# Optimization experiments

Measured on AMD Instinct MI355X. Metric: run time of the kernel, lower is better.

The kernel has to match this reference:

```python
import jax, jax.numpy as jnp
import numpy as np

D = 1024        # embed_dim
NH = 16         # num_heads
DH = D // NH    # head_dim
FFN = 2048      # ffn_hidden_dim
E = 8           # num_experts
K = 2           # top_k
B, T = 2, 1024


def setup_inputs() -> dict:
    key = jax.random.key(0)
    ks = jax.random.split(key, 6)
    s = 0.02
    return {
        "x": jax.random.normal(ks[0], (B, T, D), jnp.float32),
        "ln1_g": jnp.ones((D,), jnp.float32),
        "ln1_b": jnp.zeros((D,), jnp.float32),
        "qkv_w": jax.random.normal(ks[1], (D, 3 * D), jnp.float32) * s,   # [in,out]
        "out_w": jax.random.normal(ks[2], (D, D), jnp.float32) * s,
        "ln2_g": jnp.ones((D,), jnp.float32),
        "ln2_b": jnp.zeros((D,), jnp.float32),
        "gate_w": jax.random.normal(ks[3], (D, E), jnp.float32) * s,
        "expert_biases": jnp.zeros((E,), jnp.float32),
        "w1": jax.random.normal(ks[4], (E, D, 2 * FFN), jnp.float32) * s,  # Expert.linear1 stacked
        "w2": jax.random.normal(ks[5], (E, FFN, D), jnp.float32) * s,      # Expert.linear2 stacked
    }


def _layernorm(x, g, b, eps=1e-5):
    mu = x.mean(-1, keepdims=True)
    var = ((x - mu) ** 2).mean(-1, keepdims=True)
    return (x - mu) * jax.lax.rsqrt(var + eps) * g + b


def _rope(x, theta=10000.0):
    # x: [B, T, H, Dh]; torchtune-style interleaved (even, odd) pair rotation, input_pos=None -> 0..T-1
    Tt, Dh = x.shape[1], x.shape[3]
    inv = 1.0 / (theta ** (jnp.arange(0, Dh, 2, dtype=jnp.float32) / Dh))   # [Dh/2]
    ang = jnp.arange(Tt, dtype=jnp.float32)[:, None] * inv[None, :]         # [T, Dh/2]
    cos = jnp.cos(ang)[None, :, None, :]
    sin = jnp.sin(ang)[None, :, None, :]
    x1, x2 = x[..., 0::2], x[..., 1::2]
    return jnp.stack([x1 * cos - x2 * sin, x2 * cos + x1 * sin], axis=-1).reshape(x.shape)


def reference(x, ln1_g, ln1_b, qkv_w, out_w, ln2_g, ln2_b, gate_w, expert_biases, w1, w2):
    Bx, Tx, Dx = x.shape
    # --- attention sub-block ---
    xn = _layernorm(x, ln1_g, ln1_b)
    qkv = (xn @ qkv_w).reshape(Bx, Tx, 3, NH, DH)
    q, k, v = qkv[:, :, 0], qkv[:, :, 1], qkv[:, :, 2]
    q, k = _rope(q), _rope(k)
    q = q.transpose(0, 2, 1, 3)  # [B,H,T,Dh]
    k = k.transpose(0, 2, 1, 3)
    v = v.transpose(0, 2, 1, 3)
    scores = jnp.einsum('bhqd,bhkd->bhqk', q, k) / jnp.sqrt(jnp.float32(DH))
    attn = jax.nn.softmax(scores, axis=-1)   # non-causal (SDPA default)
    o = jnp.einsum('bhqk,bhkd->bhqd', attn, v).transpose(0, 2, 1, 3).reshape(Bx, Tx, Dx)
    x = x + o @ out_w

    # --- MoE sub-block ---
    xn2 = _layernorm(x, ln2_g, ln2_b)
    gate_scores = xn2 @ gate_w + expert_biases             # [B,T,E]
    topk_vals, topk_idx = jax.lax.top_k(gate_scores, K)    # [B,T,K]
    gates = jax.nn.softmax(topk_vals, axis=-1)             # [B,T,K]
    oh = jax.nn.one_hot(topk_idx, E, dtype=x.dtype)        # [B,T,K,E]
    comb = (oh * gates[..., None]).sum(2)                  # [B,T,E] combine weights
    # dense per-expert SwiGLU FFN (equivalent to masked dispatch: unrouted weight = 0)
    h = jnp.einsum('btd,edh->beth', xn2, w1)               # [B,E,T,2*FFN]
    h1, h2 = jnp.split(h, 2, axis=-1)
    act = jax.nn.silu(h1) * h2
    eo = jnp.einsum('beth,ehd->betd', act, w2)             # [B,E,T,D]
    ffn_out = jnp.einsum('bte,betd->btd', comb, eo)
    x = x + ffn_out

    # --- load-balancing loss ---
    usage = oh.sum((0, 1, 2))                              # [E] token counts
    usage_ratio = usage / usage.sum()
    probs = jax.nn.softmax(gate_scores, axis=-1).mean((0, 1))
    prob_ratio = probs / probs.sum()
    lb_loss = (usage_ratio * prob_ratio).sum() * E
    return x, lb_loss
```

## Files before the change

kernel.cpp:

```cpp
#include <hip/hip_runtime.h>
#include <hip/hip_fp16.h>


typedef _Float16 half8 __attribute__((ext_vector_type(8)));
typedef float f32x4 __attribute__((ext_vector_type(4)));

#define DI __device__ __forceinline__

struct Desc { int e, base, rows; };

DI float blockReduceSum(float v, float* red) {
#pragma unroll
    for (int m = 32; m; m >>= 1) v += __shfl_xor(v, m);
    int w = threadIdx.x >> 6;
    if ((threadIdx.x & 63) == 0) red[w] = v;
    __syncthreads();
    v = red[0] + red[1] + red[2] + red[3];
    __syncthreads();
    return v;
}

DI void split2(float v, __half& hi, __half& lo) {
    hi = __float2half(v);
    lo = __float2half((v - __half2float(hi)) * 2048.0f);
}

enum { EPI_RESID = 0, EPI_QKV = 1 };

template<int WM, int WN, int FM, int FN, int EPI>
__global__ __launch_bounds__(256, 2)
void k_gemm_pk(const __half* __restrict__ Ah, const __half* __restrict__ Al, int lda,
               const __half* __restrict__ Bh, const __half* __restrict__ Bl, int ldb,
               float* __restrict__ Cf, int ldc, int M, int N, int K,
               const float* __restrict__ resid,
               __half* __restrict__ qh_p, __half* __restrict__ ql_p,
               __half* __restrict__ kh_p, __half* __restrict__ kl_p,
               __half* __restrict__ vth_p, __half* __restrict__ vtl_p,
               const float* __restrict__ rc, const float* __restrict__ rs)
{
    constexpr int BM = WM * FM * 16, BN = WN * FN * 16;
    constexpr int PITCH = 40;
    __shared__ __half AsH[BM * PITCH], AsL[BM * PITCH];
    __shared__ __half BsH[BN * PITCH], BsL[BN * PITCH];
    const int tid = threadIdx.x;
    const int lane = tid & 63, w = tid >> 6;
    const int l15 = lane & 15, g = lane >> 4;
    const int wm = w / WN, wn = w % WN;
    const int m0 = blockIdx.x * BM, n0 = blockIdx.y * BN;

    f32x4 acc0[FM][FN] = {}; f32x4 acc1[FM][FN] = {};

    for (int k0 = 0; k0 < K; k0 += 32) {
        __syncthreads();
#pragma unroll
        for (int it = 0; it < BM / 64; ++it) {
            int c = it * 256 + tid, row = c >> 2, kg = c & 3;
            long src = (long)(m0 + row) * lda + k0 + kg * 8;
            *(uint4*)&AsH[row * PITCH + kg * 8] = *(const uint4*)(Ah + src);
            *(uint4*)&AsL[row * PITCH + kg * 8] = *(const uint4*)(Al + src);
        }
#pragma unroll
        for (int it = 0; it < BN / 64; ++it) {
            int c = it * 256 + tid, row = c >> 2, kg = c & 3;
            long src = (long)(n0 + row) * ldb + k0 + kg * 8;
            *(uint4*)&BsH[row * PITCH + kg * 8] = *(const uint4*)(Bh + src);
            *(uint4*)&BsL[row * PITCH + kg * 8] = *(const uint4*)(Bl + src);
        }
        __syncthreads();
        half8 ah[FM], al[FM];
#pragma unroll
        for (int i = 0; i < FM; ++i) {
            int ar = (wm * FM * 16 + i * 16 + l15) * PITCH + g * 8;
            ah[i] = *(const half8*)&AsH[ar];
            al[i] = *(const half8*)&AsL[ar];
        }
#pragma unroll
        for (int n = 0; n < FN; ++n) {
            int br = (wn * FN * 16 + n * 16 + l15) * PITCH + g * 8;
            half8 bh = *(const half8*)&BsH[br];
            half8 bl = *(const half8*)&BsL[br];
#pragma unroll
            for (int i = 0; i < FM; ++i) {
                acc0[i][n] = __builtin_amdgcn_mfma_f32_16x16x32_f16(ah[i], bh, acc0[i][n], 0, 0, 0);
                acc1[i][n] = __builtin_amdgcn_mfma_f32_16x16x32_f16(ah[i], bl, acc1[i][n], 0, 0, 0);
                acc1[i][n] = __builtin_amdgcn_mfma_f32_16x16x32_f16(al[i], bh, acc1[i][n], 0, 0, 0);
            }
        }
    }

#pragma unroll
    for (int i = 0; i < FM; ++i)
#pragma unroll
    for (int n = 0; n < FN; ++n)
#pragma unroll
    for (int j = 0; j < 4; ++j) {
        float v = acc0[i][n][j] + acc1[i][n][j] * (1.0f / 2048.0f);
        int gm = m0 + wm * FM * 16 + i * 16 + g * 4 + j;
        int gn = n0 + wn * FN * 16 + n * 16 + l15;
        if constexpr (EPI == EPI_RESID) {
            Cf[(long)gm * ldc + gn] = v + resid[(long)gm * ldc + gn];
        } else {
            int t = gm & 1023, b = gm >> 10;
            float vp = __shfl_xor(v, 1);
            if (gn < 2048) {
                int col = gn & 1023;
                int i2 = (col & 63) >> 1;
                float cv = rc[t * 32 + i2], sv = rs[t * 32 + i2];
                float rot = cv * v + sv * ((lane & 1) ? vp : -vp);
                __half hi_, lo_; split2(rot, hi_, lo_);
                long o = ((long)(b * 16 + (col >> 6)) * 1024 + t) * 64 + (col & 63);
                if (gn < 1024) { qh_p[o] = hi_; ql_p[o] = lo_; }
                else           { kh_p[o] = hi_; kl_p[o] = lo_; }
            } else {
                int col = gn - 2048;
                __half hi_, lo_; split2(v, hi_, lo_);
                long o = ((long)(b * 16 + (col >> 6)) * 64 + (col & 63)) * 1024 + t;
                vth_p[o] = hi_; vtl_p[o] = lo_;
            }
        }
    }
}

__global__ __launch_bounds__(256, 2)
void k_flash(const __half* __restrict__ qh_g, const __half* __restrict__ ql_g,
             const __half* __restrict__ kh_g, const __half* __restrict__ kl_g,
             const __half* __restrict__ vth_g, const __half* __restrict__ vtl_g,
             __half* __restrict__ oh_g, __half* __restrict__ ol_g)
{
    constexpr int P = 72;
    __shared__ __half KsH[64 * P], KsL[64 * P], VsH[64 * P], VsL[64 * P], PsH[64 * P], PsL[64 * P];
    const int tid = threadIdx.x, lane = tid & 63, w = tid >> 6;
    const int l15 = lane & 15, g = lane >> 4;
    const int q0 = blockIdx.x * 64;
    const int bh = blockIdx.y;
    const long base = (long)bh * 65536;

    half8 qhi[2], qlo[2];
    {
        long qoff = base + (long)(q0 + w * 16 + l15) * 64 + g * 8;
        qhi[0] = *(const half8*)(qh_g + qoff); qhi[1] = *(const half8*)(qh_g + qoff + 32);
        qlo[0] = *(const half8*)(ql_g + qoff); qlo[1] = *(const half8*)(ql_g + qoff + 32);
    }

    float m_[4] = {-1e30f, -1e30f, -1e30f, -1e30f};
    float l_[4] = {0.f, 0.f, 0.f, 0.f};
    f32x4 o0[4] = {}, o1[4] = {};

    for (int kt = 0; kt < 16; ++kt) {
        __syncthreads();
#pragma unroll
        for (int it = 0; it < 2; ++it) {
            int c = it * 256 + tid, row = c >> 3, kg = c & 7;
            long src = base + (long)(kt * 64 + row) * 64 + kg * 8;
            *(uint4*)&KsH[row * P + kg * 8] = *(const uint4*)(kh_g + src);
            *(uint4*)&KsL[row * P + kg * 8] = *(const uint4*)(kl_g + src);
            long vs = base + (long)row * 1024 + kt * 64 + kg * 8;
            *(uint4*)&VsH[row * P + kg * 8] = *(const uint4*)(vth_g + vs);
            *(uint4*)&VsL[row * P + kg * 8] = *(const uint4*)(vtl_g + vs);
        }
        __syncthreads();

        f32x4 s0[4] = {}, s1[4] = {};
#pragma unroll
        for (int cf = 0; cf < 4; ++cf) {
            int kr = (cf * 16 + l15) * P + g * 8;
            half8 kh0 = *(const half8*)&KsH[kr], kh1 = *(const half8*)&KsH[kr + 32];
            half8 kl0 = *(const half8*)&KsL[kr], kl1 = *(const half8*)&KsL[kr + 32];
            s0[cf] = __builtin_amdgcn_mfma_f32_16x16x32_f16(qhi[0], kh0, s0[cf], 0, 0, 0);
            s1[cf] = __builtin_amdgcn_mfma_f32_16x16x32_f16(qhi[0], kl0, s1[cf], 0, 0, 0);
            s1[cf] = __builtin_amdgcn_mfma_f32_16x16x32_f16(qlo[0], kh0, s1[cf], 0, 0, 0);
            s0[cf] = __builtin_amdgcn_mfma_f32_16x16x32_f16(qhi[1], kh1, s0[cf], 0, 0, 0);
            s1[cf] = __builtin_amdgcn_mfma_f32_16x16x32_f16(qhi[1], kl1, s1[cf], 0, 0, 0);
            s1[cf] = __builtin_amdgcn_mfma_f32_16x16x32_f16(qlo[1], kh1, s1[cf], 0, 0, 0);
        }

#pragma unroll
        for (int j = 0; j < 4; ++j) {
            float sv[4];
#pragma unroll
            for (int cf = 0; cf < 4; ++cf)
                sv[cf] = (s0[cf][j] + s1[cf][j] * (1.0f / 2048.0f)) * 0.125f;
            float mx = fmaxf(fmaxf(sv[0], sv[1]), fmaxf(sv[2], sv[3]));
#pragma unroll
            for (int msk = 8; msk; msk >>= 1) mx = fmaxf(mx, __shfl_xor(mx, msk));
            float mn = fmaxf(m_[j], mx);
            float r = expf(m_[j] - mn);
            m_[j] = mn;
            float rs = 0.f;
#pragma unroll
            for (int cf = 0; cf < 4; ++cf) {
                float p = expf(sv[cf] - mn);
                rs += p;
                __half hi_, lo_; split2(p, hi_, lo_);
                PsH[(w * 16 + g * 4 + j) * P + cf * 16 + l15] = hi_;
                PsL[(w * 16 + g * 4 + j) * P + cf * 16 + l15] = lo_;
            }
#pragma unroll
            for (int msk = 8; msk; msk >>= 1) rs += __shfl_xor(rs, msk);
            l_[j] = l_[j] * r + rs;
#pragma unroll
            for (int df = 0; df < 4; ++df) { o0[df][j] *= r; o1[df][j] *= r; }
        }
        __syncthreads();

        int pr = (w * 16 + l15) * P + g * 8;
        half8 ph0 = *(const half8*)&PsH[pr], ph1 = *(const half8*)&PsH[pr + 32];
        half8 pl0 = *(const half8*)&PsL[pr], pl1 = *(const half8*)&PsL[pr + 32];
#pragma unroll
        for (int df = 0; df < 4; ++df) {
            int vr = (df * 16 + l15) * P + g * 8;
            half8 vh0 = *(const half8*)&VsH[vr], vh1 = *(const half8*)&VsH[vr + 32];
            half8 vl0 = *(const half8*)&VsL[vr], vl1 = *(const half8*)&VsL[vr + 32];
            o0[df] = __builtin_amdgcn_mfma_f32_16x16x32_f16(ph0, vh0, o0[df], 0, 0, 0);
            o1[df] = __builtin_amdgcn_mfma_f32_16x16x32_f16(ph0, vl0, o1[df], 0, 0, 0);
            o1[df] = __builtin_amdgcn_mfma_f32_16x16x32_f16(pl0, vh0, o1[df], 0, 0, 0);
            o0[df] = __builtin_amdgcn_mfma_f32_16x16x32_f16(ph1, vh1, o0[df], 0, 0, 0);
            o1[df] = __builtin_amdgcn_mfma_f32_16x16x32_f16(ph1, vl1, o1[df], 0, 0, 0);
            o1[df] = __builtin_amdgcn_mfma_f32_16x16x32_f16(pl1, vh1, o1[df], 0, 0, 0);
        }
    }

    float invl[4];
#pragma unroll
    for (int j = 0; j < 4; ++j) invl[j] = 1.0f / l_[j];
    const int b = bh >> 4, hh = bh & 15;
#pragma unroll
    for (int df = 0; df < 4; ++df)
#pragma unroll
    for (int j = 0; j < 4; ++j) {
        float v = (o0[df][j] + o1[df][j] * (1.0f / 2048.0f)) * invl[j];
        long orow = (long)b * 1024 + q0 + w * 16 + g * 4 + j;
        int col = hh * 64 + df * 16 + l15;
        __half hi_, lo_; split2(v, hi_, lo_);
        oh_g[orow * 1024 + col] = hi_;
        ol_g[orow * 1024 + col] = lo_;
    }
}

__global__ __launch_bounds__(256) void k_wconv(const float* __restrict__ src,
                                               __half* __restrict__ dst, int R, int C)
{
    src += (long)blockIdx.z * R * C;
    dst += (long)blockIdx.z * R * C;
    __shared__ float t[64][65];
    const int tid = threadIdx.x;
    const int c0 = blockIdx.x * 64, r0 = blockIdx.y * 64;
#pragma unroll
    for (int it = 0; it < 4; ++it) {
        int idx = it * 256 + tid;
        int r = idx >> 4, c4 = (idx & 15) * 4;
        float4 v = *(const float4*)(src + (long)(r0 + r) * C + c0 + c4);
        t[r][c4] = v.x; t[r][c4 + 1] = v.y; t[r][c4 + 2] = v.z; t[r][c4 + 3] = v.w;
    }
    __syncthreads();
#pragma unroll
    for (int it = 0; it < 2; ++it) {
        int idx = it * 256 + tid;
        int orow = idx >> 3, oc = (idx & 7) * 8;
        __half v[8];
#pragma unroll
        for (int j = 0; j < 8; ++j) v[j] = __float2half(t[oc + j][orow]);
        *(uint4*)(dst + (long)(c0 + orow) * R + r0 + oc) = *(uint4*)v;
    }
}

template<bool GATHER, int MODE, int FM, int FN, int WN>
__global__ __launch_bounds__(256, 2)
void k_gemm_moe(const __half* __restrict__ A, int lda, const int* __restrict__ rowidx,
                const Desc* __restrict__ desc, const int* __restrict__ ntiles,
                const __half* __restrict__ Bbase, long sB, int ldb,
                void* __restrict__ Cv, int K)
{
    if ((int)blockIdx.x >= *ntiles) return;
    Desc d = desc[blockIdx.x];
    const __half* Bp = Bbase + (long)d.e * sB;
    constexpr int WM = 4 / WN;
    constexpr int BM = WM * FM * 16, BN = WN * FN * 16;
    constexpr int PITCH = 40;
    __shared__ __half As[BM * PITCH];
    __shared__ __half Bs[BN * PITCH];
    const int tid = threadIdx.x, lane = tid & 63, w = tid >> 6;
    const int l15 = lane & 15, g = lane >> 4;
    const int wm = w / WN, wn = w % WN;
    const int n0 = blockIdx.y * (MODE == 0 ? BN / 2 : BN);

    f32x4 acc[FM][FN] = {};
    for (int k0 = 0; k0 < K; k0 += 32) {
        __syncthreads();
#pragma unroll
        for (int it = 0; it < BM / 64; ++it) {
            int c = it * 256 + tid, row = c >> 2, kg = c & 3;
            uint4 v = make_uint4(0, 0, 0, 0);
            if constexpr (GATHER) {
                if (row < d.rows) {
                    int ar = rowidx[d.base + row];
                    v = *(const uint4*)(A + (long)ar * lda + k0 + kg * 8);
                }
            } else {
                v = *(const uint4*)(A + (long)(d.base + row) * lda + k0 + kg * 8);
            }
            *(uint4*)&As[row * PITCH + kg * 8] = v;
        }
#pragma unroll
        for (int it = 0; it < BN / 64; ++it) {
            int c = it * 256 + tid, row = c >> 2, kg = c & 3;
            int srcrow;
            if constexpr (MODE == 0) {
                int pb = row >> 4, w4 = row & 15;
                srcrow = ((pb & 1) ? 2048 : 0) + n0 + (pb >> 1) * 16 + w4;
            } else {
                srcrow = n0 + row;
            }
            *(uint4*)&Bs[row * PITCH + kg * 8] =
                *(const uint4*)(Bp + (long)srcrow * ldb + k0 + kg * 8);
        }
        __syncthreads();
        half8 a[FM];
#pragma unroll
        for (int i = 0; i < FM; ++i)
            a[i] = *(const half8*)&As[(wm * FM * 16 + i * 16 + l15) * PITCH + g * 8];
#pragma unroll
        for (int n = 0; n < FN; ++n) {
            half8 b = *(const half8*)&Bs[(wn * FN * 16 + n * 16 + l15) * PITCH + g * 8];
#pragma unroll
            for (int i = 0; i < FM; ++i)
                acc[i][n] = __builtin_amdgcn_mfma_f32_16x16x32_f16(a[i], b, acc[i][n], 0, 0, 0);
        }
    }

    if constexpr (MODE == 0) {
#pragma unroll
        for (int i = 0; i < FM; ++i)
#pragma unroll
        for (int p = 0; p < FN / 2; ++p)
#pragma unroll
        for (int j = 0; j < 4; ++j) {
            int rl = wm * FM * 16 + i * 16 + g * 4 + j;
            float h1 = acc[i][2 * p][j], h2 = acc[i][2 * p + 1][j];
            float a = h1 / (1.0f + expf(-h1)) * h2;
            if (rl >= d.rows) a = 0.0f;
            int jc = n0 + wn * (FN * 8) + p * 16 + l15;
            ((__half*)Cv)[(long)(d.base + rl) * 2048 + jc] = __float2half(a);
        }
    } else {
#pragma unroll
        for (int i = 0; i < FM; ++i)
#pragma unroll
        for (int n = 0; n < FN; ++n)
#pragma unroll
        for (int j = 0; j < 4; ++j) {
            int rl = wm * FM * 16 + i * 16 + g * 4 + j;
            int gn = n0 + wn * FN * 16 + n * 16 + l15;
            ((float*)Cv)[(long)(d.base + rl) * 1024 + gn] = acc[i][n][j];
        }
    }
}

__global__ __launch_bounds__(256) void k_transpose_pk(const float* __restrict__ src,
    __half* __restrict__ dsth, __half* __restrict__ dstl, int R, int C)
{
    __shared__ float t[64][65];
    const int tid = threadIdx.x;
    const int c0 = blockIdx.x * 64, r0 = blockIdx.y * 64;
#pragma unroll
    for (int it = 0; it < 4; ++it) {
        int idx = it * 256 + tid;
        int r = idx >> 4, c4 = (idx & 15) * 4;
        float4 v = *(const float4*)(src + (long)(r0 + r) * C + c0 + c4);
        t[r][c4] = v.x; t[r][c4 + 1] = v.y; t[r][c4 + 2] = v.z; t[r][c4 + 3] = v.w;
    }
    __syncthreads();
#pragma unroll
    for (int it = 0; it < 4; ++it) {
        int idx = it * 256 + tid;
        int orow = idx >> 4, oc = (idx & 15) * 4;
        __half hs[4], ls[4];
#pragma unroll
        for (int m = 0; m < 4; ++m) split2(t[oc + m][orow], hs[m], ls[m]);
        long o = (long)(c0 + orow) * R + r0 + oc;
        *(uint2*)&dsth[o] = *(uint2*)hs;
        *(uint2*)&dstl[o] = *(uint2*)ls;
    }
}

template<int MODE>
__global__ __launch_bounds__(256) void k_ln(const float* __restrict__ X,
    const float* __restrict__ g, const float* __restrict__ bta,
    void* __restrict__ o1, void* __restrict__ o2)
{
    __shared__ float red[4];
    const long row = blockIdx.x;
    const float* xr = X + row * 1024;
    const int c = threadIdx.x * 4;
    float4 v = *(const float4*)(xr + c);
    float mu = blockReduceSum(v.x + v.y + v.z + v.w, red) * (1.0f / 1024.0f);
    float d0 = v.x - mu, d1 = v.y - mu, d2 = v.z - mu, d3 = v.w - mu;
    float var = blockReduceSum(d0 * d0 + d1 * d1 + d2 * d2 + d3 * d3, red) * (1.0f / 1024.0f);
    float rs = 1.0f / sqrtf(var + 1e-5f);
    float4 gv = *(const float4*)(g + c);
    float4 bv = *(const float4*)(bta + c);
    float y[4] = {d0 * rs * gv.x + bv.x, d1 * rs * gv.y + bv.y,
                  d2 * rs * gv.z + bv.z, d3 * rs * gv.w + bv.w};
    if constexpr (MODE == 0) {
        __half hs[4], ls[4];
#pragma unroll
        for (int m = 0; m < 4; ++m) split2(y[m], hs[m], ls[m]);
        *(uint2*)((__half*)o1 + row * 1024 + c) = *(uint2*)hs;
        *(uint2*)((__half*)o2 + row * 1024 + c) = *(uint2*)ls;
    } else {
        *(float4*)((float*)o1 + row * 1024 + c) = make_float4(y[0], y[1], y[2], y[3]);
        __half hs[4];
#pragma unroll
        for (int m = 0; m < 4; ++m) hs[m] = __float2half(y[m]);
        *(uint2*)((__half*)o2 + row * 1024 + c) = *(uint2*)hs;
    }
}

__global__ __launch_bounds__(256) void k_rope_table(float* __restrict__ ct, float* __restrict__ st)
{
    int idx = blockIdx.x * 256 + threadIdx.x;
    int t = idx >> 5, i = idx & 31;
    float inv = 1.0f / (float)pow(10000.0, (double)i / 32.0);
    float ang = (float)t * inv;
    ct[idx] = cosf(ang);
    st[idx] = sinf(ang);
}

__global__ __launch_bounds__(256) void k_gate(const float* __restrict__ xn2,
    const float* __restrict__ gw, const float* __restrict__ eb,
    int* __restrict__ topidx, float* __restrict__ gates,
    float* __restrict__ pprob)
{
    __shared__ float pp[4][8];
    const int lane = threadIdx.x & 63, w = threadIdx.x >> 6;
    const int t = blockIdx.x * 4 + w;
    const float* xr = xn2 + (long)t * 1024;
    float sc[8] = {0, 0, 0, 0, 0, 0, 0, 0};
#pragma unroll
    for (int i = 0; i < 4; ++i) {
        int d = i * 256 + lane * 4;
        float4 xv = *(const float4*)(xr + d);
        float xa[4] = {xv.x, xv.y, xv.z, xv.w};
#pragma unroll
        for (int j = 0; j < 4; ++j) {
            float xx = xa[j];
            const float4* gp = (const float4*)(gw + (long)(d + j) * 8);
            float4 g0 = gp[0], g1 = gp[1];
            sc[0] += xx * g0.x; sc[1] += xx * g0.y; sc[2] += xx * g0.z; sc[3] += xx * g0.w;
            sc[4] += xx * g1.x; sc[5] += xx * g1.y; sc[6] += xx * g1.z; sc[7] += xx * g1.w;
        }
    }
#pragma unroll
    for (int e = 0; e < 8; ++e) {
#pragma unroll
        for (int m = 32; m; m >>= 1) sc[e] += __shfl_xor(sc[e], m);
        sc[e] += eb[e];
    }
    if (lane == 0) {
        int i1 = 0; float v1 = sc[0];
        for (int e = 1; e < 8; ++e) if (sc[e] > v1) { v1 = sc[e]; i1 = e; }
        int i2 = (i1 == 0) ? 1 : 0; float v2 = sc[i2];
        for (int e = 0; e < 8; ++e) if (e != i1 && sc[e] > v2) { v2 = sc[e]; i2 = e; }
        float e2 = expf(v2 - v1);
        gates[t * 2] = 1.0f / (1.0f + e2);
        gates[t * 2 + 1] = e2 / (1.0f + e2);
        topidx[t * 2] = i1; topidx[t * 2 + 1] = i2;
        float mxx = sc[0];
        for (int e = 1; e < 8; ++e) mxx = fmaxf(mxx, sc[e]);
        float se = 0.0f, pe[8];
        for (int e = 0; e < 8; ++e) { pe[e] = expf(sc[e] - mxx); se += pe[e]; }
        float inv = 1.0f / se;
        for (int e = 0; e < 8; ++e) pp[w][e] = pe[e] * inv;
    }
    __syncthreads();
    if (threadIdx.x < 8)
        pprob[(long)blockIdx.x * 8 + threadIdx.x] =
            pp[0][threadIdx.x] + pp[1][threadIdx.x] + pp[2][threadIdx.x] + pp[3][threadIdx.x];
}

__global__ __launch_bounds__(256) void k_route(const int* __restrict__ topidx,
    int* __restrict__ rowidx, int* __restrict__ invpos,
    int* __restrict__ ntiles, Desc* __restrict__ desc, int* __restrict__ cnt)
{
    __shared__ int cnt_s[8], base_s[8], fill[8];
    const int tid = threadIdx.x;
    if (tid < 8) { cnt_s[tid] = 0; fill[tid] = 0; }
    __syncthreads();
    for (int i = tid; i < 4096; i += 256)
        atomicAdd(&cnt_s[topidx[i]], 1);
    __syncthreads();
    if (tid == 0) {
        int tl[8]; int running = 0, maxT = 0;
        for (int e = 0; e < 8; ++e) {
            int ce = cnt_s[e];
            cnt[e] = ce;
            base_s[e] = running;
            tl[e] = (ce + 127) >> 7;
            running += tl[e] * 128;
            if (tl[e] > maxT) maxT = tl[e];
        }
        int nt = 0;
        for (int r = 0; r < maxT; ++r)
            for (int e = 0; e < 8; ++e)
                if (r < tl[e]) {
                    desc[nt].e = e;
                    desc[nt].base = base_s[e] + r * 128;
                    desc[nt].rows = min(128, cnt_s[e] - r * 128);
                    ++nt;
                }
        *ntiles = nt;
    }
    __syncthreads();
    for (int t = tid; t < 2048; t += 256) {
#pragma unroll
        for (int s = 0; s < 2; ++s) {
            int e = topidx[t * 2 + s];
            int p = base_s[e] + atomicAdd(&fill[e], 1);
            rowidx[p] = t;
            invpos[t * 2 + s] = p;
        }
    }
}

__global__ __launch_bounds__(256) void k_combine(const float* __restrict__ x1,
    const float* __restrict__ eo, const int* __restrict__ invpos,
    const float* __restrict__ gates, float* __restrict__ out)
{
    const int t = blockIdx.x, c = threadIdx.x * 4;
    float g0 = gates[t * 2], g1 = gates[t * 2 + 1];
    int p0 = invpos[t * 2], p1 = invpos[t * 2 + 1];
    float4 xv = *(const float4*)(x1 + (long)t * 1024 + c);
    float4 e0 = *(const float4*)(eo + (long)p0 * 1024 + c);
    float4 e1 = *(const float4*)(eo + (long)p1 * 1024 + c);
    float4 o;
    o.x = xv.x + g0 * e0.x + g1 * e1.x;
    o.y = xv.y + g0 * e0.y + g1 * e1.y;
    o.z = xv.z + g0 * e0.z + g1 * e1.z;
    o.w = xv.w + g0 * e0.w + g1 * e1.w;
    *(float4*)(out + (long)t * 1024 + c) = o;
}

__global__ __launch_bounds__(256) void k_loss(const int* __restrict__ cnt,
    const float* __restrict__ pprob, float* __restrict__ out)
{
    __shared__ float m[32][8];
    const int tid = threadIdx.x;
    const int e = tid & 7, g = tid >> 3;
    float local = 0.0f;
    for (int b = g; b < 512; b += 32) local += pprob[b * 8 + e];
    m[g][e] = local;
    __syncthreads();
    if (tid == 0) {
        float us = 0, ps = 0, pe[8], ue[8];
        for (int ee = 0; ee < 8; ++ee) {
            float s = 0;
            for (int gg = 0; gg < 32; ++gg) s += m[gg][ee];
            pe[ee] = s; ps += s;
            ue[ee] = (float)cnt[ee]; us += ue[ee];
        }
        float lb = 0;
        for (int ee = 0; ee < 8; ++ee) lb += (ue[ee] / us) * (pe[ee] / ps);
        out[2097152] = lb * 8.0f;
    }
}

extern "C" void kernel_launch(void* const* d_in, const int* in_sizes, int n_in,
                              void* d_out, int out_size, void* d_ws, size_t ws_size,
                              hipStream_t stream)
{
    const float* x    = (const float*)d_in[0];
    const float* ln1g = (const float*)d_in[1];
    const float* ln1b = (const float*)d_in[2];
    const float* qkvw = (const float*)d_in[3];
    const float* outw = (const float*)d_in[4];
    const float* ln2g = (const float*)d_in[5];
    const float* ln2b = (const float*)d_in[6];
    const float* gw   = (const float*)d_in[7];
    const float* eb   = (const float*)d_in[8];
    const float* w1   = (const float*)d_in[9];
    const float* w2   = (const float*)d_in[10];
    float* out = (float*)d_out;
    char* ws = (char*)d_ws;

    constexpr size_t OFF_QWTH = 0;
    constexpr size_t OFF_QWTL = 6291456;
    constexpr size_t OFF_OWTH = 12582912;
    constexpr size_t OFF_OWTL = 14680064;
    constexpr size_t OFF_XN1H = 16777216;
    constexpr size_t OFF_XN1L = 20971520;
    constexpr size_t OFF_QH   = 25165824;
    constexpr size_t OFF_QL   = 29360128;
    constexpr size_t OFF_KH   = 33554432;
    constexpr size_t OFF_KL   = 37748736;
    constexpr size_t OFF_VTH  = 41943040;
    constexpr size_t OFF_VTL  = 46137344;
    constexpr size_t OFF_OH   = 50331648;
    constexpr size_t OFF_OL   = 54525952;
    constexpr size_t OFF_X1   = 58720256;
    constexpr size_t OFF_XN2F = 67108864;
    constexpr size_t OFF_XN2H = 75497472;
    constexpr size_t OFF_RC   = 79691776;
    constexpr size_t OFF_RS   = 79822848;
    constexpr size_t OFF_IDX  = 79953920;
    constexpr size_t OFF_GATES= 79970304;
    constexpr size_t OFF_INVP = 79986688;
    constexpr size_t OFF_ROWI = 80003072;
    constexpr size_t OFF_CNT  = 80023552;
    constexpr size_t OFF_NT   = 80023616;
    constexpr size_t OFF_DESC = 80023680;
    constexpr size_t OFF_PPROB= 80024704;
    constexpr size_t OFF_ACT  = 80041984;
    constexpr size_t OFF_EO   = 101013504;
    constexpr size_t OFF_W1T  = 121985024;
    constexpr size_t OFF_W2T  = 189093888;

    __half* qwth = (__half*)(ws + OFF_QWTH);
    __half* qwtl = (__half*)(ws + OFF_QWTL);
    __half* owth = (__half*)(ws + OFF_OWTH);
    __half* owtl = (__half*)(ws + OFF_OWTL);
    __half* xn1h = (__half*)(ws + OFF_XN1H);
    __half* xn1l = (__half*)(ws + OFF_XN1L);
    __half* qh   = (__half*)(ws + OFF_QH);
    __half* ql   = (__half*)(ws + OFF_QL);
    __half* kh   = (__half*)(ws + OFF_KH);
    __half* kl   = (__half*)(ws + OFF_KL);
    __half* vth  = (__half*)(ws + OFF_VTH);
    __half* vtl  = (__half*)(ws + OFF_VTL);
    __half* oh   = (__half*)(ws + OFF_OH);
    __half* ol   = (__half*)(ws + OFF_OL);
    float* x1    = (float*)(ws + OFF_X1);
    float* xn2f  = (float*)(ws + OFF_XN2F);
    __half* xn2h = (__half*)(ws + OFF_XN2H);
    float* rc    = (float*)(ws + OFF_RC);
    float* rs    = (float*)(ws + OFF_RS);
    int*   idx   = (int*)(ws + OFF_IDX);
    float* gates = (float*)(ws + OFF_GATES);
    int*   invp  = (int*)(ws + OFF_INVP);
    int*   rowi  = (int*)(ws + OFF_ROWI);
    int*   cnt   = (int*)(ws + OFF_CNT);
    int*   nt    = (int*)(ws + OFF_NT);
    Desc*  desc  = (Desc*)(ws + OFF_DESC);
    float* pprob = (float*)(ws + OFF_PPROB);
    __half* act  = (__half*)(ws + OFF_ACT);
    float* eo    = (float*)(ws + OFF_EO);
    __half* w1t  = (__half*)(ws + OFF_W1T);
    __half* w2t  = (__half*)(ws + OFF_W2T);

    k_transpose_pk<<<dim3(48, 16, 1), 256, 0, stream>>>(qkvw, qwth, qwtl, 1024, 3072);
    k_transpose_pk<<<dim3(16, 16, 1), 256, 0, stream>>>(outw, owth, owtl, 1024, 1024);
    k_wconv<<<dim3(64, 16, 8), 256, 0, stream>>>(w1, w1t, 1024, 4096);
    k_wconv<<<dim3(16, 32, 8), 256, 0, stream>>>(w2, w2t, 2048, 1024);
    k_rope_table<<<dim3(128), 256, 0, stream>>>(rc, rs);

    k_ln<0><<<dim3(2048), 256, 0, stream>>>(x, ln1g, ln1b, xn1h, xn1l);

    k_gemm_pk<2, 2, 2, 4, EPI_QKV><<<dim3(32, 24, 1), 256, 0, stream>>>(
        xn1h, xn1l, 1024, qwth, qwtl, 1024, nullptr, 0, 2048, 3072, 1024,
        nullptr, qh, ql, kh, kl, vth, vtl, rc, rs);

    k_flash<<<dim3(16, 32, 1), 256, 0, stream>>>(qh, ql, kh, kl, vth, vtl, oh, ol);

    k_gemm_pk<2, 2, 2, 2, EPI_RESID><<<dim3(32, 16, 1), 256, 0, stream>>>(
        oh, ol, 1024, owth, owtl, 1024, x1, 1024, 2048, 1024, 1024,
        x, nullptr, nullptr, nullptr, nullptr, nullptr, nullptr, nullptr, nullptr);

    k_ln<1><<<dim3(2048), 256, 0, stream>>>(x1, ln2g, ln2b, xn2f, xn2h);

    k_gate<<<dim3(512), 256, 0, stream>>>(xn2f, gw, eb, idx, gates, pprob);
    k_route<<<dim3(1), 256, 0, stream>>>(idx, rowi, invp, nt, desc, cnt);

    k_gemm_moe<true, 0, 4, 4, 2><<<dim3(40, 32, 1), 256, 0, stream>>>(
        xn2h, 1024, rowi, desc, nt, w1t, 4194304, 1024, act, 1024);

    k_gemm_moe<false, 1, 2, 4, 1><<<dim3(40, 16, 1), 256, 0, stream>>>(
        act, 2048, nullptr, desc, nt, w2t, 2097152, 2048, eo, 2048);

    k_combine<<<dim3(2048), 256, 0, stream>>>(x1, eo, invp, gates, out);
    k_loss<<<dim3(1), 256, 0, stream>>>(cnt, pprob, out);
}
```

Before: 411.2 us.

## Register-prefetch next K tile in GEMM and MoE kernels to overlap global loads

Both the split-precision GEMM and the MoE grouped GEMM now precompute per-thread source pointers and LDS destinations once, and keep the next K-slice in registers. Each iteration stores the prefetched registers to LDS, issues global loads for the following slice, then waits only on LDS (lgkmcnt) before the barrier, so global latency overlaps the MFMA work. For the gather path this also hoists the rowidx lookup out of the K loop. It costs extra VGPRs for the staging registers, which may hurt occupancy under launch_bounds(256,2), and it relies on raw s_barrier with manual waitcnt.

```diff
diff --git a/kernel.cpp b/kernel.cpp
--- a/kernel.cpp
+++ b/kernel.cpp
@@ -6,6 +6,8 @@
 typedef float f32x4 __attribute__((ext_vector_type(4)));
 
 #define DI __device__ __forceinline__
+#define BARRIER() asm volatile("s_barrier" ::: "memory")
+#define WAIT_LGKM0() asm volatile("s_waitcnt lgkmcnt(0)" ::: "memory")
 
 struct Desc { int e, base, rows; };
 
@@ -40,6 +42,7 @@
 {
     constexpr int BM = WM * FM * 16, BN = WN * FN * 16;
     constexpr int PITCH = 40;
+    constexpr int AIT = BM / 64, BIT = BN / 64;
     __shared__ __half AsH[BM * PITCH], AsL[BM * PITCH];
     __shared__ __half BsH[BN * PITCH], BsL[BN * PITCH];
     const int tid = threadIdx.x;
@@ -48,25 +51,64 @@
     const int wm = w / WN, wn = w % WN;
     const int m0 = blockIdx.x * BM, n0 = blockIdx.y * BN;
 
+    const __half *pAh[AIT], *pAl[AIT], *pBh[BIT], *pBl[BIT];
+    int adst[AIT], bdst[BIT];
+#pragma unroll
+    for (int it = 0; it < AIT; ++it) {
+        int c = it * 256 + tid, row = c >> 2, kg = c & 3;
+        long src = (long)(m0 + row) * lda + kg * 8;
+        pAh[it] = Ah + src; pAl[it] = Al + src;
+        adst[it] = row * PITCH + kg * 8;
+    }
+#pragma unroll
+    for (int it = 0; it < BIT; ++it) {
+        int c = it * 256 + tid, row = c >> 2, kg = c & 3;
+        long src = (long)(n0 + row) * ldb + kg * 8;
+        pBh[it] = Bh + src; pBl[it] = Bl + src;
+        bdst[it] = row * PITCH + kg * 8;
+    }
+
+    uint4 rAh[AIT], rAl[AIT], rBh[BIT], rBl[BIT];
+#pragma unroll
+    for (int it = 0; it < AIT; ++it) {
+        rAh[it] = *(const uint4*)(pAh[it]);
+        rAl[it] = *(const uint4*)(pAl[it]);
+    }
+#pragma unroll
+    for (int it = 0; it < BIT; ++it) {
+        rBh[it] = *(const uint4*)(pBh[it]);
+        rBl[it] = *(const uint4*)(pBl[it]);
+    }
+
     f32x4 acc0[FM][FN] = {}; f32x4 acc1[FM][FN] = {};
 
     for (int k0 = 0; k0 < K; k0 += 32) {
-        __syncthreads();
-#pragma unroll
-        for (int it = 0; it < BM / 64; ++it) {
-            int c = it * 256 + tid, row = c >> 2, kg = c & 3;
-            long src = (long)(m0 + row) * lda + k0 + kg * 8;
-            *(uint4*)&AsH[row * PITCH + kg * 8] = *(const uint4*)(Ah + src);
-            *(uint4*)&AsL[row * PITCH + kg * 8] = *(const uint4*)(Al + src);
-        }
-#pragma unroll
-        for (int it = 0; it < BN / 64; ++it) {
-            int c = it * 256 + tid, row = c >> 2, kg = c & 3;
-            long src = (long)(n0 + row) * ldb + k0 + kg * 8;
-            *(uint4*)&BsH[row * PITCH + kg * 8] = *(const uint4*)(Bh + src);
-            *(uint4*)&BsL[row * PITCH + kg * 8] = *(const uint4*)(Bl + src);
-        }
-        __syncthreads();
+        BARRIER();
+#pragma unroll
+        for (int it = 0; it < AIT; ++it) {
+            *(uint4*)&AsH[adst[it]] = rAh[it];
+            *(uint4*)&AsL[adst[it]] = rAl[it];
+        }
+#pragma unroll
+        for (int it = 0; it < BIT; ++it) {
+            *(uint4*)&BsH[bdst[it]] = rBh[it];
+            *(uint4*)&BsL[bdst[it]] = rBl[it];
+        }
+        if (k0 + 32 < K) {
+#pragma unroll
+            for (int it = 0; it < AIT; ++it) {
+                rAh[it] = *(const uint4*)(pAh[it] + k0 + 32);
+                rAl[it] = *(const uint4*)(pAl[it] + k0 + 32);
+            }
+#pragma unroll
+            for (int it = 0; it < BIT; ++it) {
+                rBh[it] = *(const uint4*)(pBh[it] + k0 + 32);
+                rBl[it] = *(const uint4*)(pBl[it] + k0 + 32);
+            }
+        }
+        WAIT_LGKM0();
+        BARRIER();
+
         half8 ah[FM], al[FM];
 #pragma unroll
         for (int i = 0; i < FM; ++i) {
@@ -276,6 +318,7 @@
     const __half* Bp = Bbase + (long)d.e * sB;
     constexpr int WM = 4 / WN;
     constexpr int BM = WM * FM * 16, BN = WN * FN * 16;
+    constexpr int AIT = BM / 64, BIT = BN / 64;
     constexpr int PITCH = 40;
     __shared__ __half As[BM * PITCH];
     __shared__ __half Bs[BN * PITCH];
@@ -284,37 +327,61 @@
     const int wm = w / WN, wn = w % WN;
     const int n0 = blockIdx.y * (MODE == 0 ? BN / 2 : BN);
 
+    const __half* pA[AIT]; bool aval[AIT]; int adst[AIT];
+    const __half* pB[BIT]; int bdst[BIT];
+#pragma unroll
+    for (int it = 0; it < AIT; ++it) {
+        int c = it * 256 + tid, row = c >> 2, kg = c & 3;
+        adst[it] = row * PITCH + kg * 8;
+        if constexpr (GATHER) {
+            aval[it] = row < d.rows;
+            int ar = aval[it] ? rowidx[d.base + row] : 0;
+            pA[it] = A + (long)ar * lda + kg * 8;
+        } else {
+            aval[it] = true;
+            pA[it] = A + (long)(d.base + row) * lda + kg * 8;
+        }
+    }
+#pragma unroll
+    for (int it = 0; it < BIT; ++it) {
+        int c = it * 256 + tid, row = c >> 2, kg = c & 3;
+        bdst[it] = row * PITCH + kg * 8;
+        int srcrow;
+        if constexpr (MODE == 0) {
+            int pb = row >> 4, w4 = row & 15;
+            srcrow = ((pb & 1) ? 2048 : 0) + n0 + (pb >> 1) * 16 + w4;
+        } else {
+            srcrow = n0 + row;
+        }
+        pB[it] = Bp + (long)srcrow * ldb + kg * 8;
+    }
+
+    uint4 rA[AIT], rB[BIT];
+#pragma unroll
+    for (int it = 0; it < AIT; ++it)
+        rA[it] = aval[it] ? *(const uint4*)(pA[it]) : make_uint4(0, 0, 0, 0);
+#pragma unroll
+    for (int it = 0; it < BIT; ++it)
+        rB[it] = *(const uint4*)(pB[it]);
+
     f32x4 acc[FM][FN] = {};
     for (int k0 = 0; k0 < K; k0 += 32) {
-        __syncthreads();
-#pragma unroll
-        for (int it = 0; it < BM / 64; ++it) {
-            int c = it * 256 + tid, row = c >> 2, kg = c & 3;
-            uint4 v = make_uint4(0, 0, 0, 0);
-            if constexpr (GATHER) {
-                if (row < d.rows) {
-                    int ar = rowidx[d.base + row];
-                    v = *(const uint4*)(A + (long)ar * lda + k0 + kg * 8);
-                }
-            } else {
-                v = *(const uint4*)(A + (long)(d.base + row) * lda + k0 + kg * 8);
-            }
-            *(uint4*)&As[row * PITCH + kg * 8] = v;
-        }
-#pragma unroll
-        for (int it = 0; it < BN / 64; ++it) {
-            int c = it * 256 + tid, row = c >> 2, kg = c & 3;
-            int srcrow;
-            if constexpr (MODE == 0) {
-                int pb = row >> 4, w4 = row & 15;
-                srcrow = ((pb & 1) ? 2048 : 0) + n0 + (pb >> 1) * 16 + w4;
-            } else {
-                srcrow = n0 + row;
-            }
-            *(uint4*)&Bs[row * PITCH + kg * 8] =
-                *(const uint4*)(Bp + (long)srcrow * ldb + k0 + kg * 8);
-        }
-        __syncthreads();
+        BARRIER();
+#pragma unroll
+        for (int it = 0; it < AIT; ++it) *(uint4*)&As[adst[it]] = rA[it];
+#pragma unroll
+        for (int it = 0; it < BIT; ++it) *(uint4*)&Bs[bdst[it]] = rB[it];
+        if (k0 + 32 < K) {
+#pragma unroll
+            for (int it = 0; it < AIT; ++it)
+                rA[it] = aval[it] ? *(const uint4*)(pA[it] + k0 + 32) : make_uint4(0, 0, 0, 0);
+#pragma unroll
+            for (int it = 0; it < BIT; ++it)
+                rB[it] = *(const uint4*)(pB[it] + k0 + 32);
+        }
+        WAIT_LGKM0();
+        BARRIER();
+
         half8 a[FM];
 #pragma unroll
         for (int i = 0; i < FM; ++i)
```

Result: slower. 524.4 us (+27.6%).

## Prefetch next K-tile into registers in MoE GEMM and hoist address math

Applied to the files above, without the earlier changes.

Restructures the MoE GEMM main loop so the global loads for the next K-slice are issued into registers before the current slice's MFMAs run, giving register-level double buffering. Gather row indices and source addresses are computed once before the loop instead of every iteration. __syncthreads is replaced by raw s_barrier plus an explicit lgkmcnt wait, so the barrier no longer waits on outstanding global loads. This costs extra VGPRs for the staged tiles and pointers, which may lower occupancy under launch_bounds(256,2).

```diff
diff --git a/kernel.cpp b/kernel.cpp
--- a/kernel.cpp
+++ b/kernel.cpp
@@ -6,6 +6,8 @@
 typedef float f32x4 __attribute__((ext_vector_type(4)));
 
 #define DI __device__ __forceinline__
+#define BARRIER() asm volatile("s_barrier" ::: "memory")
+#define WAIT_LGKM0() asm volatile("s_waitcnt lgkmcnt(0)" ::: "memory")
 
 struct Desc { int e, base, rows; };
 
@@ -276,6 +278,7 @@
     const __half* Bp = Bbase + (long)d.e * sB;
     constexpr int WM = 4 / WN;
     constexpr int BM = WM * FM * 16, BN = WN * FN * 16;
+    constexpr int AIT = BM / 64, BIT = BN / 64;
     constexpr int PITCH = 40;
     __shared__ __half As[BM * PITCH];
     __shared__ __half Bs[BN * PITCH];
@@ -284,37 +287,61 @@
     const int wm = w / WN, wn = w % WN;
     const int n0 = blockIdx.y * (MODE == 0 ? BN / 2 : BN);
 
+    const __half* pA[AIT]; bool aval[AIT]; int adst[AIT];
+    const __half* pB[BIT]; int bdst[BIT];
+#pragma unroll
+    for (int it = 0; it < AIT; ++it) {
+        int c = it * 256 + tid, row = c >> 2, kg = c & 3;
+        adst[it] = row * PITCH + kg * 8;
+        if constexpr (GATHER) {
+            aval[it] = row < d.rows;
+            int ar = aval[it] ? rowidx[d.base + row] : 0;
+            pA[it] = A + (long)ar * lda + kg * 8;
+        } else {
+            aval[it] = true;
+            pA[it] = A + (long)(d.base + row) * lda + kg * 8;
+        }
+    }
+#pragma unroll
+    for (int it = 0; it < BIT; ++it) {
+        int c = it * 256 + tid, row = c >> 2, kg = c & 3;
+        bdst[it] = row * PITCH + kg * 8;
+        int srcrow;
+        if constexpr (MODE == 0) {
+            int pb = row >> 4, w4 = row & 15;
+            srcrow = ((pb & 1) ? 2048 : 0) + n0 + (pb >> 1) * 16 + w4;
+        } else {
+            srcrow = n0 + row;
+        }
+        pB[it] = Bp + (long)srcrow * ldb + kg * 8;
+    }
+
+    uint4 rA[AIT], rB[BIT];
+#pragma unroll
+    for (int it = 0; it < AIT; ++it)
+        rA[it] = aval[it] ? *(const uint4*)(pA[it]) : make_uint4(0, 0, 0, 0);
+#pragma unroll
+    for (int it = 0; it < BIT; ++it)
+        rB[it] = *(const uint4*)(pB[it]);
+
     f32x4 acc[FM][FN] = {};
     for (int k0 = 0; k0 < K; k0 += 32) {
-        __syncthreads();
-#pragma unroll
-        for (int it = 0; it < BM / 64; ++it) {
-            int c = it * 256 + tid, row = c >> 2, kg = c & 3;
-            uint4 v = make_uint4(0, 0, 0, 0);
-            if constexpr (GATHER) {
-                if (row < d.rows) {
-                    int ar = rowidx[d.base + row];
-                    v = *(const uint4*)(A + (long)ar * lda + k0 + kg * 8);
-                }
-            } else {
-                v = *(const uint4*)(A + (long)(d.base + row) * lda + k0 + kg * 8);
-            }
-            *(uint4*)&As[row * PITCH + kg * 8] = v;
-        }
-#pragma unroll
-        for (int it = 0; it < BN / 64; ++it) {
-            int c = it * 256 + tid, row = c >> 2, kg = c & 3;
-            int srcrow;
-            if constexpr (MODE == 0) {
-                int pb = row >> 4, w4 = row & 15;
-                srcrow = ((pb & 1) ? 2048 : 0) + n0 + (pb >> 1) * 16 + w4;
-            } else {
-                srcrow = n0 + row;
-            }
-            *(uint4*)&Bs[row * PITCH + kg * 8] =
-                *(const uint4*)(Bp + (long)srcrow * ldb + k0 + kg * 8);
-        }
-        __syncthreads();
+        BARRIER();
+#pragma unroll
+        for (int it = 0; it < AIT; ++it) *(uint4*)&As[adst[it]] = rA[it];
+#pragma unroll
+        for (int it = 0; it < BIT; ++it) *(uint4*)&Bs[bdst[it]] = rB[it];
+        if (k0 + 32 < K) {
+#pragma unroll
+            for (int it = 0; it < AIT; ++it)
+                rA[it] = aval[it] ? *(const uint4*)(pA[it] + k0 + 32) : make_uint4(0, 0, 0, 0);
+#pragma unroll
+            for (int it = 0; it < BIT; ++it)
+                rB[it] = *(const uint4*)(pB[it] + k0 + 32);
+        }
+        WAIT_LGKM0();
+        BARRIER();
+
         half8 a[FM];
 #pragma unroll
         for (int i = 0; i < FM; ++i)
```

Result: slower. 449.4 us (+9.3%).

## Use direct global-to-LDS loads with XOR swizzle in MoE expert GEMMs

Applied to the files above, without the earlier changes.

The MoE GEMM tile loads now use global_load_lds, writing straight into LDS instead of staging through registers. Padded LDS rows are replaced by an unpadded layout with an XOR swizzle to avoid bank conflicts, and row addresses are precomputed once per block. Invalid gathered rows now read from a zeroed scratch region (xn1h, memset after the QKV GEMM), and launch bounds rise to 4 blocks per CU. The aim is lower register pressure, less load overhead and higher occupancy, at the cost of an extra memset and reliance on a reused buffer staying zero.

```diff
diff --git a/kernel.cpp b/kernel.cpp
--- a/kernel.cpp
+++ b/kernel.cpp
@@ -265,45 +265,45 @@
 }
 
 template<bool GATHER, int MODE, int FM, int FN, int WN>
-__global__ __launch_bounds__(256, 2)
+__global__ __launch_bounds__(256, 4)
 void k_gemm_moe(const __half* __restrict__ A, int lda, const int* __restrict__ rowidx,
                 const Desc* __restrict__ desc, const int* __restrict__ ntiles,
                 const __half* __restrict__ Bbase, long sB, int ldb,
-                void* __restrict__ Cv, int K)
+                void* __restrict__ Cv, int K, const __half* __restrict__ zp)
 {
     if ((int)blockIdx.x >= *ntiles) return;
     Desc d = desc[blockIdx.x];
     const __half* Bp = Bbase + (long)d.e * sB;
     constexpr int WM = 4 / WN;
     constexpr int BM = WM * FM * 16, BN = WN * FN * 16;
-    constexpr int PITCH = 40;
-    __shared__ __half As[BM * PITCH];
-    __shared__ __half Bs[BN * PITCH];
+    constexpr int ACH = BM / 16, BCH = BN / 16;
+    constexpr int CPW = (ACH + BCH) / 4;
+    __shared__ __half As[BM * 32];
+    __shared__ __half Bs[BN * 32];
     const int tid = threadIdx.x, lane = tid & 63, w = tid >> 6;
     const int l15 = lane & 15, g = lane >> 4;
     const int wm = w / WN, wn = w % WN;
     const int n0 = blockIdx.y * (MODE == 0 ? BN / 2 : BN);
 
-    f32x4 acc[FM][FN] = {};
-    for (int k0 = 0; k0 < K; k0 += 32) {
-        __syncthreads();
-#pragma unroll
-        for (int it = 0; it < BM / 64; ++it) {
-            int c = it * 256 + tid, row = c >> 2, kg = c & 3;
-            uint4 v = make_uint4(0, 0, 0, 0);
+    const int dlt = lane >> 2;
+    const int kgs = ((lane & 3) ^ ((lane >> 3) & 3)) * 8;
+    const __half* src[CPW];
+    __half* ldst[CPW];
+#pragma unroll
+    for (int ci = 0; ci < CPW; ++ci) {
+        int chunk = w * CPW + ci;
+        if (chunk < ACH) {
+            int row = chunk * 16 + dlt;
+            ldst[ci] = &As[chunk * 512];
             if constexpr (GATHER) {
-                if (row < d.rows) {
-                    int ar = rowidx[d.base + row];
-                    v = *(const uint4*)(A + (long)ar * lda + k0 + kg * 8);
-                }
+                bool valid = row < d.rows;
+                int ar = valid ? rowidx[d.base + row] : 0;
+                src[ci] = valid ? (A + (long)ar * lda + kgs) : (zp + kgs);
             } else {
-                v = *(const uint4*)(A + (long)(d.base + row) * lda + k0 + kg * 8);
+                src[ci] = A + (long)(d.base + row) * lda + kgs;
             }
-            *(uint4*)&As[row * PITCH + kg * 8] = v;
-        }
-#pragma unroll
-        for (int it = 0; it < BN / 64; ++it) {
-            int c = it * 256 + tid, row = c >> 2, kg = c & 3;
+        } else {
+            int row = (chunk - ACH) * 16 + dlt;
             int srcrow;
             if constexpr (MODE == 0) {
                 int pb = row >> 4, w4 = row & 15;
@@ -311,17 +311,29 @@
             } else {
                 srcrow = n0 + row;
             }
-            *(uint4*)&Bs[row * PITCH + kg * 8] =
-                *(const uint4*)(Bp + (long)srcrow * ldb + k0 + kg * 8);
-        }
+            ldst[ci] = &Bs[(chunk - ACH) * 512];
+            src[ci] = Bp + (long)srcrow * ldb + kgs;
+        }
+    }
+
+    const int sg = (g ^ ((l15 >> 1) & 3)) * 8;
+
+    f32x4 acc[FM][FN] = {};
+    for (int k0 = 0; k0 < K; k0 += 32) {
         __syncthreads();
+#pragma unroll
+        for (int ci = 0; ci < CPW; ++ci)
+            __builtin_amdgcn_global_load_lds((const void*)(src[ci] + k0),
+                                             (void*)ldst[ci], 16, 0, 0);
+        __syncthreads();
+
         half8 a[FM];
 #pragma unroll
         for (int i = 0; i < FM; ++i)
-            a[i] = *(const half8*)&As[(wm * FM * 16 + i * 16 + l15) * PITCH + g * 8];
+            a[i] = *(const half8*)&As[(wm * FM * 16 + i * 16 + l15) * 32 + sg];
 #pragma unroll
         for (int n = 0; n < FN; ++n) {
-            half8 b = *(const half8*)&Bs[(wn * FN * 16 + n * 16 + l15) * PITCH + g * 8];
+            half8 b = *(const half8*)&Bs[(wn * FN * 16 + n * 16 + l15) * 32 + sg];
 #pragma unroll
             for (int i = 0; i < FM; ++i)
                 acc[i][n] = __builtin_amdgcn_mfma_f32_16x16x32_f16(a[i], b, acc[i][n], 0, 0, 0);
@@ -645,6 +657,7 @@
     float* eo    = (float*)(ws + OFF_EO);
     __half* w1t  = (__half*)(ws + OFF_W1T);
     __half* w2t  = (__half*)(ws + OFF_W2T);
+    __half* zp   = xn1h;
 
     k_transpose_pk<<<dim3(48, 16, 1), 256, 0, stream>>>(qkvw, qwth, qwtl, 1024, 3072);
     k_transpose_pk<<<dim3(16, 16, 1), 256, 0, stream>>>(outw, owth, owtl, 1024, 1024);
@@ -658,6 +671,8 @@
         xn1h, xn1l, 1024, qwth, qwtl, 1024, nullptr, 0, 2048, 3072, 1024,
         nullptr, qh, ql, kh, kl, vth, vtl, rc, rs);
 
+    hipMemsetAsync(zp, 0, 4096, stream);
+
     k_flash<<<dim3(16, 32, 1), 256, 0, stream>>>(qh, ql, kh, kl, vth, vtl, oh, ol);
 
     k_gemm_pk<2, 2, 2, 2, EPI_RESID><<<dim3(32, 16, 1), 256, 0, stream>>>(
@@ -670,10 +685,10 @@
     k_route<<<dim3(1), 256, 0, stream>>>(idx, rowi, invp, nt, desc, cnt);
 
     k_gemm_moe<true, 0, 4, 4, 2><<<dim3(40, 32, 1), 256, 0, stream>>>(
-        xn2h, 1024, rowi, desc, nt, w1t, 4194304, 1024, act, 1024);
+        xn2h, 1024, rowi, desc, nt, w1t, 4194304, 1024, act, 1024, zp);
 
     k_gemm_moe<false, 1, 2, 4, 1><<<dim3(40, 16, 1), 256, 0, stream>>>(
-        act, 2048, nullptr, desc, nt, w2t, 2097152, 2048, eo, 2048);
+        act, 2048, nullptr, desc, nt, w2t, 2097152, 2048, eo, 2048, zp);
 
     k_combine<<<dim3(2048), 256, 0, stream>>>(x1, eo, invp, gates, out);
     k_loss<<<dim3(1), 256, 0, stream>>>(cnt, pprob, out);
```

After: 383.5 us. 6.7% less time.
